# Optimization experiments

Hardware: AMD Instinct MI355X
Metric: run time of the kernel (lower is better)

The kernel has to match this reference:

```python
import jax, jax.numpy as jnp
import numpy as np
from math import sqrt

B, P, D = 4, 2048, 1024
H, DK = 16, 64  # n_heads, d_keys


def setup_inputs() -> dict:
    key = jax.random.key(0)
    ks = jax.random.split(key, 6)
    s = 1.0 / sqrt(D)
    return {
        "target_embedding": jax.random.normal(ks[0], (B, P, D), dtype=jnp.float32),
        "Wq": jax.random.normal(ks[1], (D, H * DK), dtype=jnp.float32) * s,
        "bq": jnp.zeros((H * DK,), dtype=jnp.float32),
        "Wk": jax.random.normal(ks[2], (D, H * DK), dtype=jnp.float32) * s,
        "bk": jnp.zeros((H * DK,), dtype=jnp.float32),
        "Wv": jax.random.normal(ks[3], (D, H * DK), dtype=jnp.float32) * s,
        "bv": jnp.zeros((H * DK,), dtype=jnp.float32),
        "Wo": jax.random.normal(ks[4], (H * DK, D), dtype=jnp.float32) * s,
        "bo": jnp.zeros((D,), dtype=jnp.float32),
    }


def reference(target_embedding, Wq, bq, Wk, bk, Wv, bv, Wo, bo):
    x = target_embedding
    b, p, _ = x.shape
    # QKV projections -> [B, P, H, DK]
    q = (x @ Wq + bq).reshape(b, p, H, DK)
    k = (x @ Wk + bk).reshape(b, p, H, DK)
    v = (x @ Wv + bv).reshape(b, p, H, DK)
    scale = 1.0 / sqrt(DK)
    scores = jnp.einsum("bphd,bqhd->bhpq", q, k)  # [B, H, P, P]
    A = jax.nn.softmax(scale * scores, axis=-1)  # dropout is identity in eval
    rep = jnp.einsum("bhpq,bqhd->bphd", A, v).reshape(b, p, H * DK)
    return rep @ Wo + bo
```

## Files before the change

kernel.cpp:

```cpp
#include <hip/hip_runtime.h>

typedef __attribute__((ext_vector_type(8))) short short8;
typedef __attribute__((ext_vector_type(4))) short short4v;
typedef __attribute__((ext_vector_type(4))) float f32x4;
typedef __attribute__((ext_vector_type(4))) unsigned short ushort4v;
typedef __attribute__((ext_vector_type(2))) unsigned int uint2v;

#define GLOBAL_AS __attribute__((address_space(1)))
#define LDS_AS    __attribute__((address_space(3)))

__device__ __forceinline__ unsigned short f2bf(float f) {
    unsigned int u = __float_as_uint(f);
    u += 0x7fffu + ((u >> 16) & 1u);
    return (unsigned short)(u >> 16);
}

__device__ __forceinline__ unsigned int pack_rhu(float a, float b) {
    unsigned int ua = __float_as_uint(a) + 0x8000u;
    unsigned int ub = __float_as_uint(b) + 0x8000u;
    return __builtin_amdgcn_perm(ub, ua, 0x07060302u);
}

__device__ __forceinline__ short4v pack4_rhu(float p0, float p1, float p2, float p3) {
    uint2v uu;
    uu[0] = pack_rhu(p0, p1);
    uu[1] = pack_rhu(p2, p3);
    return __builtin_bit_cast(short4v, uu);
}

__device__ __forceinline__ float fexp2(float x) {
    return __builtin_amdgcn_exp2f(x);
}

__device__ __forceinline__ void async_cp16(void* lds, const void* g) {
    __builtin_amdgcn_global_load_lds((GLOBAL_AS unsigned int*)g,
                                     (LDS_AS unsigned int*)lds, 16, 0, 0);
}

#define SCL2E 0.18033688011112042591999058512524f

__global__ void prep_kernel(const float* __restrict__ X,
                            const float* __restrict__ Wq,
                            const float* __restrict__ Wk,
                            const float* __restrict__ Wv,
                            const float* __restrict__ Wo,
                            unsigned short* __restrict__ Xb,
                            unsigned short* __restrict__ Wts) {
    const int z = blockIdx.z;
    if (z < 4) {
        __shared__ float tile[32][33];
        const float* src = (z == 0) ? Wq : (z == 1) ? Wk : (z == 2) ? Wv : Wo;
        unsigned short* dst = Wts + z * 1048576;
        const int tx = threadIdx.x, ty = threadIdx.y;
        const int x0 = blockIdx.x * 32, y0 = blockIdx.y * 32;
#pragma unroll
        for (int i = 0; i < 32; i += 8)
            tile[ty + i][tx] = src[(y0 + ty + i) * 1024 + x0 + tx];
        __syncthreads();
#pragma unroll
        for (int i = 0; i < 32; i += 8)
            dst[(x0 + ty + i) * 1024 + y0 + tx] = f2bf(tile[tx][ty + i]);
    } else {
        const int tid = threadIdx.y * 32 + threadIdx.x;
        const int chunk = blockIdx.y * 32 + blockIdx.x;
        const int base = chunk * 8192;
#pragma unroll
        for (int pass = 0; pass < 8; ++pass) {
            int i = base + pass * 1024 + tid * 4;
            float4 v = *(const float4*)&X[i];
            ushort4v o;
            o.x = f2bf(v.x); o.y = f2bf(v.y); o.z = f2bf(v.z); o.w = f2bf(v.w);
            *(ushort4v*)&Xb[i] = o;
        }
    }
}

__device__ __forceinline__ void gemm_stage_tile(
    const unsigned short* __restrict__ A, const unsigned short* __restrict__ Bt,
    int m0, int n0, int k0, int tid, unsigned short* Asb, unsigned short* Bsb) {
#pragma unroll
    for (int i = 0; i < 2; ++i) {
        int s = tid + 256 * i;
        int r = s >> 2, gp = s & 3;
        int g = gp ^ ((r >> 1) & 3);
        async_cp16(&Asb[s * 8], &A[(m0 + r) * 1024 + k0 + g * 8]);
    }
#pragma unroll
    for (int i = 0; i < 2; ++i) {
        int s = tid + 256 * i;
        int r = s >> 2, gp = s & 3;
        int g = gp ^ ((r >> 1) & 3);
        async_cp16(&Bsb[s * 8], &Bt[(n0 + r) * 1024 + k0 + g * 8]);
    }
}

__device__ __forceinline__ void gemm_mainloop_128(
    const unsigned short* __restrict__ A, const unsigned short* __restrict__ Bt,
    int m0, int n0, unsigned short* As, unsigned short* Bs, f32x4 acc[4][4]) {
    const int tid = threadIdx.x;
    const int lane = tid & 63;
    const int wave = tid >> 6;
    const int wr = wave >> 1, wc = wave & 1;
    const int c = lane & 15, quad = lane >> 4;

#pragma unroll
    for (int mt = 0; mt < 4; ++mt)
#pragma unroll
        for (int nt = 0; nt < 4; ++nt)
            acc[mt][nt] = (f32x4)0.0f;

    gemm_stage_tile(A, Bt, m0, n0, 0, tid, As, Bs);

    for (int k0 = 0; k0 < 1024; k0 += 32) {
        const int cur = (k0 >> 5) & 1;
        unsigned short* Asb = As + cur * 4096;
        unsigned short* Bsb = Bs + cur * 4096;
        asm volatile("s_waitcnt vmcnt(0)" ::: "memory");
        __syncthreads();
        if (k0 + 32 < 1024)
            gemm_stage_tile(A, Bt, m0, n0, k0 + 32, tid,
                            As + (cur ^ 1) * 4096, Bs + (cur ^ 1) * 4096);

        short8 af[4], bf[4];
#pragma unroll
        for (int mt = 0; mt < 4; ++mt) {
            int r = wr * 64 + mt * 16 + c;
            int gp = quad ^ ((r >> 1) & 3);
            af[mt] = *(const short8*)&Asb[r * 32 + gp * 8];
        }
#pragma unroll
        for (int nt = 0; nt < 4; ++nt) {
            int r = wc * 64 + nt * 16 + c;
            int gp = quad ^ ((r >> 1) & 3);
            bf[nt] = *(const short8*)&Bsb[r * 32 + gp * 8];
        }
#pragma unroll
        for (int mt = 0; mt < 4; ++mt)
#pragma unroll
            for (int nt = 0; nt < 4; ++nt)
                acc[mt][nt] = __builtin_amdgcn_mfma_f32_16x16x32_bf16(
                    af[mt], bf[nt], acc[mt][nt], 0, 0, 0);
    }
}

__global__ __launch_bounds__(256, 3) void gemm_qkv_kernel(
    const unsigned short* __restrict__ Xb, const unsigned short* __restrict__ Wts,
    const float* __restrict__ bq, const float* __restrict__ bk,
    const float* __restrict__ bv, unsigned short* __restrict__ Qb,
    unsigned short* __restrict__ Kb, unsigned short* __restrict__ Vtb) {
    __shared__ __align__(16) unsigned short As[2 * 128 * 32];
    __shared__ __align__(16) unsigned short Bs[2 * 128 * 32];
    const int z = blockIdx.z;
    const unsigned short* Wz = Wts + z * 1048576;
    const bool swapped = (z == 2);
    const int m0 = (swapped ? blockIdx.x : blockIdx.y) * 128;
    const int n0 = (swapped ? blockIdx.y : blockIdx.x) * 128;
    const unsigned short* Amat = swapped ? Wz : Xb;
    const unsigned short* Bmat = swapped ? Xb : Wz;
    f32x4 acc[4][4];
    gemm_mainloop_128(Amat, Bmat, m0, n0, As, Bs, acc);

    const int lane = threadIdx.x & 63, wave = threadIdx.x >> 6;
    const int wr = wave >> 1, wc = wave & 1;
    const int c = lane & 15, quad = lane >> 4;

    if (!swapped) {
        const float* bias = (z == 0) ? bq : bk;
        unsigned short* dst = (z == 0) ? Qb : Kb;
        const float qscale = (z == 0) ? SCL2E : 1.0f;
#pragma unroll
        for (int nt = 0; nt < 4; ++nt) {
            int col = n0 + wc * 64 + nt * 16 + c;
            float bb = bias[col];
            int h = col >> 6, dk = col & 63;
#pragma unroll
            for (int mt = 0; mt < 4; ++mt) {
#pragma unroll
                for (int r = 0; r < 4; ++r) {
                    int row = m0 + wr * 64 + mt * 16 + quad * 4 + r;
                    int b = row >> 11, p = row & 2047;
                    float v = (acc[mt][nt][r] + bb) * qscale;
                    dst[((b * 16 + h) * 2048 + p) * 64 + dk] = f2bf(v);
                }
            }
        }
    } else {
        float bb2[4][4];
#pragma unroll
        for (int mt = 0; mt < 4; ++mt)
#pragma unroll
            for (int r = 0; r < 4; ++r)
                bb2[mt][r] = bv[m0 + wr * 64 + mt * 16 + quad * 4 + r];
#pragma unroll
        for (int nt = 0; nt < 4; ++nt) {
            int colp = n0 + wc * 64 + nt * 16 + c;
            int b = colp >> 11, p = colp & 2047;
#pragma unroll
            for (int mt = 0; mt < 4; ++mt) {
#pragma unroll
                for (int r = 0; r < 4; ++r) {
                    int rowv = m0 + wr * 64 + mt * 16 + quad * 4 + r;
                    int h = rowv >> 6, dk = rowv & 63;
                    float v = acc[mt][nt][r] + bb2[mt][r];
                    Vtb[(b * 16 + h) * 131072 + dk * 2048 + p] = f2bf(v);
                }
            }
        }
    }
}

__device__ __forceinline__ void load_kv_regs(
    const unsigned short* __restrict__ Kbh, const unsigned short* __restrict__ Vbh,
    int k0, int tid, short8 kr[2], short8 vr[2]) {
#pragma unroll
    for (int i = 0; i < 2; ++i) {
        int s = tid + 256 * i;
        int r = s >> 3, gp = s & 7;
        int g = gp ^ (r & 7);
        kr[i] = *(const short8*)&Kbh[(k0 + r) * 64 + g * 8];
        vr[i] = *(const short8*)&Vbh[r * 2048 + k0 + gp * 8];
    }
}

__global__ __launch_bounds__(256, 2) void attn_kernel(
    const unsigned short* __restrict__ Q, const unsigned short* __restrict__ K,
    const unsigned short* __restrict__ Vt, unsigned short* __restrict__ rep) {
    __shared__ __align__(16) unsigned short SMEM[17408];
    const int tid = threadIdx.x, lane = tid & 63, wave = tid >> 6;
    const int c = lane & 15, quad = lane >> 4;
    const int bh = blockIdx.y;
    const int q0 = blockIdx.x * 256 + wave * 64;
    const unsigned short* Qbh = Q + bh * (2048 * 64);
    const unsigned short* Kbh = K + bh * (2048 * 64);
    const unsigned short* Vbh = Vt + bh * (64 * 2048);

    short8 qf[4][2];
#pragma unroll
    for (int t = 0; t < 4; ++t)
#pragma unroll
        for (int ks = 0; ks < 2; ++ks)
            qf[t][ks] = *(const short8*)&Qbh[(q0 + t * 16 + c) * 64 + ks * 32 + quad * 8];

    short8 kr[2], vr[2];
    load_kv_regs(Kbh, Vbh, 0, tid, kr, vr);

    f32x4 o[4][4];
    float lpart[4] = {0.0f, 0.0f, 0.0f, 0.0f};
#pragma unroll
    for (int t = 0; t < 4; ++t)
#pragma unroll
        for (int d = 0; d < 4; ++d) o[t][d] = (f32x4)0.0f;

    for (int it = 0; it < 32; ++it) {
        const int buf = it & 1;
        unsigned short* Ksb = &SMEM[buf * 4096];
        unsigned short* Vsb = &SMEM[8192 + buf * 4608];
#pragma unroll
        for (int i = 0; i < 2; ++i) {
            int s = tid + 256 * i;
            int r = s >> 3, gp = s & 7;
            *(short8*)&Ksb[s * 8] = kr[i];
            *(short8*)&Vsb[r * 72 + gp * 8] = vr[i];
        }
        __syncthreads();
        if (it < 31)
            load_kv_regs(Kbh, Vbh, (it + 1) * 64, tid, kr, vr);

        short8 kf[4][2];
#pragma unroll
        for (int nt = 0; nt < 4; ++nt)
#pragma unroll
            for (int ks = 0; ks < 2; ++ks) {
                int r = nt * 16 + c;
                int gp2 = (quad + 4 * ks) ^ (r & 7);
                kf[nt][ks] = *(const short8*)&Ksb[r * 64 + gp2 * 8];
            }

        short4v vf[4][4];
#pragma unroll
        for (int dkt = 0; dkt < 4; ++dkt) {
            int r = dkt * 16 + c;
#pragma unroll
            for (int kt = 0; kt < 4; ++kt)
                vf[dkt][kt] = *(const short4v*)&Vsb[r * 72 + kt * 16 + quad * 4];
        }

        f32x4 zc = (f32x4)0.0f;
        zc = __builtin_amdgcn_mfma_f32_16x16x32_bf16(kf[0][0], qf[0][0], zc, 0, 0, 0);
        zc = __builtin_amdgcn_mfma_f32_16x16x32_bf16(kf[0][1], qf[0][1], zc, 0, 0, 0);
#pragma unroll
        for (int u = 0; u < 16; ++u) {
            const int t = u >> 2, nt = u & 3;
            f32x4 zn = (f32x4)0.0f;
            if (u < 15) {
                const int t2 = (u + 1) >> 2, nt2 = (u + 1) & 3;
                zn = __builtin_amdgcn_mfma_f32_16x16x32_bf16(kf[nt2][0], qf[t2][0], zn, 0, 0, 0);
                zn = __builtin_amdgcn_mfma_f32_16x16x32_bf16(kf[nt2][1], qf[t2][1], zn, 0, 0, 0);
            }
            float p0 = fexp2(zc[0]), p1 = fexp2(zc[1]);
            float p2 = fexp2(zc[2]), p3 = fexp2(zc[3]);
            lpart[t] += (p0 + p1) + (p2 + p3);
            short4v pf = pack4_rhu(p0, p1, p2, p3);
#pragma unroll
            for (int dkt = 0; dkt < 4; ++dkt)
                o[t][dkt] = __builtin_amdgcn_mfma_f32_16x16x16bf16_1k(
                    vf[dkt][nt], pf, o[t][dkt], 0, 0, 0);
            zc = zn;
        }
    }

    float inv[4];
#pragma unroll
    for (int t = 0; t < 4; ++t) {
        float l = lpart[t];
        l += __shfl_xor(l, 16);
        l += __shfl_xor(l, 32);
        inv[t] = 1.0f / l;
    }

    __syncthreads();
    const int b = bh >> 4, h = bh & 15;
    unsigned short* ob = &SMEM[wave * 2304];
#pragma unroll
    for (int pass = 0; pass < 2; ++pass) {
#pragma unroll
        for (int th = 0; th < 2; ++th) {
            int t = pass * 2 + th;
#pragma unroll
            for (int dkt = 0; dkt < 4; ++dkt) {
                short4v frag = pack4_rhu(o[t][dkt][0] * inv[t], o[t][dkt][1] * inv[t],
                                         o[t][dkt][2] * inv[t], o[t][dkt][3] * inv[t]);
                *(short4v*)&ob[(th * 16 + c) * 72 + dkt * 16 + quad * 4] = frag;
            }
        }
        asm volatile("s_waitcnt lgkmcnt(0)" ::: "memory");
#pragma unroll
        for (int sp = 0; sp < 4; ++sp) {
            int qr = sp * 8 + (lane >> 3);
            int d8 = (lane & 7) * 8;
            short8 row = *(const short8*)&ob[qr * 72 + d8];
            *(short8*)&rep[(b * 2048 + q0 + pass * 32 + qr) * 1024 + h * 64 + d8] = row;
        }
    }
}

__global__ __launch_bounds__(256, 3) void gemm_out_kernel(
    const unsigned short* __restrict__ rep, const unsigned short* __restrict__ Wot,
    const float* __restrict__ bo, float* __restrict__ out) {
    __shared__ __align__(16) unsigned short As[2 * 128 * 32];
    __shared__ __align__(16) unsigned short Bs[2 * 128 * 32];
    const int m0 = blockIdx.y * 128, n0 = blockIdx.x * 128;
    f32x4 acc[4][4];
    gemm_mainloop_128(rep, Wot, m0, n0, As, Bs, acc);
    const int lane = threadIdx.x & 63, wave = threadIdx.x >> 6;
    const int wr = wave >> 1, wc = wave & 1;
    const int c = lane & 15, quad = lane >> 4;
#pragma unroll
    for (int nt = 0; nt < 4; ++nt) {
        int col = n0 + wc * 64 + nt * 16 + c;
        float bb = bo[col];
#pragma unroll
        for (int mt = 0; mt < 4; ++mt) {
            int row = m0 + wr * 64 + mt * 16 + quad * 4;
#pragma unroll
            for (int r = 0; r < 4; ++r)
                out[(row + r) * 1024 + col] = acc[mt][nt][r] + bb;
        }
    }
}

extern "C" void kernel_launch(void* const* d_in, const int* in_sizes, int n_in,
                              void* d_out, int out_size, void* d_ws, size_t ws_size,
                              hipStream_t stream) {
    (void)in_sizes; (void)n_in; (void)out_size; (void)ws_size;
    const float* X  = (const float*)d_in[0];
    const float* Wq = (const float*)d_in[1];
    const float* bq = (const float*)d_in[2];
    const float* Wk = (const float*)d_in[3];
    const float* bk = (const float*)d_in[4];
    const float* Wv = (const float*)d_in[5];
    const float* bv = (const float*)d_in[6];
    const float* Wo = (const float*)d_in[7];
    const float* bo = (const float*)d_in[8];
    float* out = (float*)d_out;

    char* ws = (char*)d_ws;
    unsigned short* Xb   = (unsigned short*)(ws);
    unsigned short* Wts  = (unsigned short*)(ws + (16u << 20));
    unsigned short* Qb   = (unsigned short*)(ws + (24u << 20));
    unsigned short* Kb   = (unsigned short*)(ws + (40u << 20));
    unsigned short* Vtb  = (unsigned short*)(ws + (56u << 20));
    unsigned short* repb = (unsigned short*)(ws);

    prep_kernel<<<dim3(32, 32, 5), dim3(32, 8), 0, stream>>>(X, Wq, Wk, Wv, Wo, Xb, Wts);
    gemm_qkv_kernel<<<dim3(8, 64, 3), 256, 0, stream>>>(Xb, Wts, bq, bk, bv, Qb, Kb, Vtb);
    attn_kernel<<<dim3(8, 64), 256, 0, stream>>>(Qb, Kb, Vtb, repb);
    gemm_out_kernel<<<dim3(8, 64), 256, 0, stream>>>(repb, Wts + 3 * 1048576, bo, out);
}
```

Before: 290.4 us.

## Triple-buffer GEMM mainloop and stage Q/K epilogue through LDS for vector stores

The shared GEMM mainloop moves from double to triple buffering with a prefetch distance of two k-tiles, waiting only on the older tile's loads (vmcnt(4)), so global loads overlap more compute. The QKV kernel now always computes W^T·X^T orientation, and Q/K results are transposed through an LDS tile so each thread writes 16-byte vector stores instead of scattered 2-byte stores. LDS per block grows to 48KB, which may cut occupancy below the 3 blocks per CU set in launch bounds. The grid mapping for z<2 also changes and relies on the launch configuration matching.

```diff
diff --git a/kernel.cpp b/kernel.cpp
--- a/kernel.cpp
+++ b/kernel.cpp
@@ -84,24 +84,20 @@
         int r = s >> 2, gp = s & 3;
         int g = gp ^ ((r >> 1) & 3);
         async_cp16(&Asb[s * 8], &A[(m0 + r) * 1024 + k0 + g * 8]);
-    }
-#pragma unroll
-    for (int i = 0; i < 2; ++i) {
-        int s = tid + 256 * i;
-        int r = s >> 2, gp = s & 3;
-        int g = gp ^ ((r >> 1) & 3);
         async_cp16(&Bsb[s * 8], &Bt[(n0 + r) * 1024 + k0 + g * 8]);
     }
 }
 
 __device__ __forceinline__ void gemm_mainloop_128(
     const unsigned short* __restrict__ A, const unsigned short* __restrict__ Bt,
-    int m0, int n0, unsigned short* As, unsigned short* Bs, f32x4 acc[4][4]) {
+    int m0, int n0, unsigned short* GS, f32x4 acc[4][4]) {
     const int tid = threadIdx.x;
     const int lane = tid & 63;
     const int wave = tid >> 6;
     const int wr = wave >> 1, wc = wave & 1;
     const int c = lane & 15, quad = lane >> 4;
+    unsigned short* As = GS;
+    unsigned short* Bs = GS + 12288;
 
 #pragma unroll
     for (int mt = 0; mt < 4; ++mt)
@@ -110,16 +106,23 @@
             acc[mt][nt] = (f32x4)0.0f;
 
     gemm_stage_tile(A, Bt, m0, n0, 0, tid, As, Bs);
-
+    gemm_stage_tile(A, Bt, m0, n0, 32, tid, As + 4096, Bs + 4096);
+
+    int bufc = 0;
     for (int k0 = 0; k0 < 1024; k0 += 32) {
-        const int cur = (k0 >> 5) & 1;
-        unsigned short* Asb = As + cur * 4096;
-        unsigned short* Bsb = Bs + cur * 4096;
-        asm volatile("s_waitcnt vmcnt(0)" ::: "memory");
+        unsigned short* Asb = As + bufc * 4096;
+        unsigned short* Bsb = Bs + bufc * 4096;
+        if (k0 < 992) {
+            asm volatile("s_waitcnt vmcnt(4)" ::: "memory");
+        } else {
+            asm volatile("s_waitcnt vmcnt(0)" ::: "memory");
+        }
         __syncthreads();
-        if (k0 + 32 < 1024)
-            gemm_stage_tile(A, Bt, m0, n0, k0 + 32, tid,
-                            As + (cur ^ 1) * 4096, Bs + (cur ^ 1) * 4096);
+        if (k0 + 64 < 1024) {
+            int nb = bufc + 2; if (nb >= 3) nb -= 3;
+            gemm_stage_tile(A, Bt, m0, n0, k0 + 64, tid,
+                            As + nb * 4096, Bs + nb * 4096);
+        }
 
         short8 af[4], bf[4];
 #pragma unroll
@@ -140,6 +143,7 @@
             for (int nt = 0; nt < 4; ++nt)
                 acc[mt][nt] = __builtin_amdgcn_mfma_f32_16x16x32_bf16(
                     af[mt], bf[nt], acc[mt][nt], 0, 0, 0);
+        bufc = (bufc == 2) ? 0 : bufc + 1;
     }
 }
 
@@ -148,41 +152,51 @@
     const float* __restrict__ bq, const float* __restrict__ bk,
     const float* __restrict__ bv, unsigned short* __restrict__ Qb,
     unsigned short* __restrict__ Kb, unsigned short* __restrict__ Vtb) {
-    __shared__ __align__(16) unsigned short As[2 * 128 * 32];
-    __shared__ __align__(16) unsigned short Bs[2 * 128 * 32];
+    __shared__ __align__(16) unsigned short GS[24576];
     const int z = blockIdx.z;
     const unsigned short* Wz = Wts + z * 1048576;
-    const bool swapped = (z == 2);
-    const int m0 = (swapped ? blockIdx.x : blockIdx.y) * 128;
-    const int n0 = (swapped ? blockIdx.y : blockIdx.x) * 128;
-    const unsigned short* Amat = swapped ? Wz : Xb;
-    const unsigned short* Bmat = swapped ? Xb : Wz;
+    const int m0 = blockIdx.x * 128;
+    const int n0 = blockIdx.y * 128;
     f32x4 acc[4][4];
-    gemm_mainloop_128(Amat, Bmat, m0, n0, As, Bs, acc);
+    gemm_mainloop_128(Wz, Xb, m0, n0, GS, acc);
 
     const int lane = threadIdx.x & 63, wave = threadIdx.x >> 6;
     const int wr = wave >> 1, wc = wave & 1;
     const int c = lane & 15, quad = lane >> 4;
 
-    if (!swapped) {
+    if (z < 2) {
         const float* bias = (z == 0) ? bq : bk;
         unsigned short* dst = (z == 0) ? Qb : Kb;
-        const float qscale = (z == 0) ? SCL2E : 1.0f;
-#pragma unroll
-        for (int nt = 0; nt < 4; ++nt) {
-            int col = n0 + wc * 64 + nt * 16 + c;
-            float bb = bias[col];
-            int h = col >> 6, dk = col & 63;
-#pragma unroll
-            for (int mt = 0; mt < 4; ++mt) {
-#pragma unroll
-                for (int r = 0; r < 4; ++r) {
-                    int row = m0 + wr * 64 + mt * 16 + quad * 4 + r;
-                    int b = row >> 11, p = row & 2047;
-                    float v = (acc[mt][nt][r] + bb) * qscale;
-                    dst[((b * 16 + h) * 2048 + p) * 64 + dk] = f2bf(v);
-                }
+        const float qs = (z == 0) ? SCL2E : 1.0f;
+        __syncthreads();
+        unsigned short* TILE = GS;
+#pragma unroll
+        for (int mt = 0; mt < 4; ++mt) {
+            int ocb = m0 + wr * 64 + mt * 16 + quad * 4;
+            float b0 = bias[ocb + 0], b1 = bias[ocb + 1];
+            float b2 = bias[ocb + 2], b3 = bias[ocb + 3];
+#pragma unroll
+            for (int nt = 0; nt < 4; ++nt) {
+                int pl = wc * 64 + nt * 16 + c;
+                int dkl = wr * 64 + mt * 16 + quad * 4;
+                short4v frag = pack4_rhu((acc[mt][nt][0] + b0) * qs,
+                                         (acc[mt][nt][1] + b1) * qs,
+                                         (acc[mt][nt][2] + b2) * qs,
+                                         (acc[mt][nt][3] + b3) * qs);
+                *(short4v*)&TILE[pl * 136 + dkl] = frag;
             }
+        }
+        __syncthreads();
+        const int hbase = m0 >> 6;
+#pragma unroll
+        for (int pass = 0; pass < 32; ++pass) {
+            int pl = pass * 4 + (lane >> 4);
+            int dkl8 = (lane & 15) * 8;
+            short8 v = *(const short8*)&TILE[pl * 136 + dkl8];
+            int pp = n0 + pl;
+            int b = pp >> 11, p = pp & 2047;
+            int h = hbase + (dkl8 >> 6), dk = dkl8 & 63;
+            *(short8*)&dst[((b * 16 + h) * 2048 + p) * 64 + dk] = v;
         }
     } else {
         float bb2[4][4];
@@ -347,11 +361,10 @@
 __global__ __launch_bounds__(256, 3) void gemm_out_kernel(
     const unsigned short* __restrict__ rep, const unsigned short* __restrict__ Wot,
     const float* __restrict__ bo, float* __restrict__ out) {
-    __shared__ __align__(16) unsigned short As[2 * 128 * 32];
-    __shared__ __align__(16) unsigned short Bs[2 * 128 * 32];
+    __shared__ __align__(16) unsigned short GS[24576];
     const int m0 = blockIdx.y * 128, n0 = blockIdx.x * 128;
     f32x4 acc[4][4];
-    gemm_mainloop_128(rep, Wot, m0, n0, As, Bs, acc);
+    gemm_mainloop_128(rep, Wot, m0, n0, GS, acc);
     const int lane = threadIdx.x & 63, wave = threadIdx.x >> 6;
     const int wr = wave >> 1, wc = wave & 1;
     const int c = lane & 15, quad = lane >> 4;
```

New measurement: 296.6 us. 1.02x slower.
